# Performance work log

Hardware: AMD Instinct MI355X
Metric: run time of the kernel (lower is better)

Reference implementation:

```python
import jax, jax.numpy as jnp
import numpy as np

WIDTH = 66   # channel width; width*SX*SY == 2376 (hardcoded GRU input size)
SX, SY = 6, 6
MODES = 3
HID = 16     # GRU hidden; forced by self.out = Linear(16, 1)
FEAT = WIDTH * SX * SY  # 2376
EPS = 1e-5   # InstanceNorm2d eps


def _gelu(x):
    return jax.nn.gelu(x, approximate=False)  # torch default exact gelu


def _inorm(x):
    # InstanceNorm2d, affine=False, biased variance over spatial dims
    m = x.mean(axis=(-2, -1), keepdims=True)
    v = ((x - m) ** 2).mean(axis=(-2, -1), keepdims=True)
    return (x - m) * jax.lax.rsqrt(v + EPS)


def _conv1x1(x, w, b):
    # x: [n, ci, h, w], w: [co, ci], b: [co]
    return jnp.einsum('bixy,oi->boxy', x, w) + b[None, :, None, None]


def _mlp(x, wa, ba, wb, bb):
    return _conv1x1(_gelu(_conv1x1(x, wa, ba)), wb, bb)


def _spectral(x, w1r, w1i, w2r, w2i):
    # x: [n, c, SX, SY]
    w1 = w1r + 1j * w1i
    w2 = w2r + 1j * w2i
    xft = jnp.fft.rfft2(x)  # [n, c, SX, SY//2+1]
    o1 = jnp.einsum('bixy,ioxy->boxy', xft[:, :, :MODES, :MODES], w1)
    o2 = jnp.einsum('bixy,ioxy->boxy', xft[:, :, SX - MODES:, :MODES], w2)
    oft = jnp.zeros((x.shape[0], w1.shape[1], SX, SY // 2 + 1), dtype=xft.dtype)
    oft = oft.at[:, :, :MODES, :MODES].set(o1)
    oft = oft.at[:, :, SX - MODES:, :MODES].set(o2)
    return jnp.fft.irfft2(oft, s=(SX, SY))


def _gru_layer(x, wi, wh, bi, bh):
    # x: [T, B, I]; torch GRU gate order: r, z, n
    B = x.shape[1]
    H = wh.shape[1]

    def step(h, xt):
        gi = xt @ wi.T + bi
        gh = h @ wh.T + bh
        ir, iz, inn = jnp.split(gi, 3, axis=-1)
        hr, hz, hn = jnp.split(gh, 3, axis=-1)
        r = jax.nn.sigmoid(ir + hr)
        z = jax.nn.sigmoid(iz + hz)
        n = jnp.tanh(inn + r * hn)
        h_new = (1.0 - z) * n + z * h
        return h_new, h_new

    h0 = jnp.zeros((B, H), x.dtype)
    _, ys = jax.lax.scan(step, h0, x)
    return ys  # [T, B, H]


def setup_inputs() -> dict:
    key = jax.random.key(0)
    ks = iter(jax.random.split(key, 64))
    W = WIDTH
    scale = 1.0 / (W * W)

    def n(shape, s=0.02):
        return (jax.random.normal(next(ks), shape, dtype=jnp.float32) * s)

    def spec(shape):
        return scale * jax.random.uniform(next(ks), shape, dtype=jnp.float32)

    inp = {
        'X': jax.random.normal(next(ks), (64, 256, SX, SY), dtype=jnp.float32),
        'p_w': n((3, W), 0.3), 'p_b': n((W,)),
        'c0_w1r': spec((W, W, MODES, MODES)), 'c0_w1i': spec((W, W, MODES, MODES)),
        'c0_w2r': spec((W, W, MODES, MODES)), 'c0_w2i': spec((W, W, MODES, MODES)),
        'c1_w1r': spec((W, W, MODES, MODES)), 'c1_w1i': spec((W, W, MODES, MODES)),
        'c1_w2r': spec((W, W, MODES, MODES)), 'c1_w2i': spec((W, W, MODES, MODES)),
        'm0a_w': n((W, W)), 'm0a_b': n((W,)), 'm0b_w': n((W, W)), 'm0b_b': n((W,)),
        'm1a_w': n((W, W)), 'm1a_b': n((W,)), 'm1b_w': n((W, W)), 'm1b_b': n((W,)),
        'w0_w': n((W, W)), 'w0_b': n((W,)),
        'w1_w': n((W, W)), 'w1_b': n((W,)),
        'gru0_wi': n((3 * HID, FEAT)), 'gru0_wh': n((3 * HID, HID)),
        'gru0_bi': n((3 * HID,)), 'gru0_bh': n((3 * HID,)),
        'gru1_wi': n((3 * HID, HID)), 'gru1_wh': n((3 * HID, HID)),
        'gru1_bi': n((3 * HID,)), 'gru1_bh': n((3 * HID,)),
        'out_w': n((1, HID)), 'out_b': n((1,)),
    }
    return inp


def reference(X, p_w, p_b,
              c0_w1r, c0_w1i, c0_w2r, c0_w2i,
              c1_w1r, c1_w1i, c1_w2r, c1_w2i,
              m0a_w, m0a_b, m0b_w, m0b_b,
              m1a_w, m1a_b, m1b_w, m1b_b,
              w0_w, w0_b, w1_w, w1_b,
              gru0_wi, gru0_wh, gru0_bi, gru0_bh,
              gru1_wi, gru1_wh, gru1_bi, gru1_bh,
              out_w, out_b):
    B, T = X.shape[0], X.shape[1]
    N = B * T
    x = (X + 0.01).reshape(N, SX, SY)
    # grid channels (linspace 0..1)
    gx = jnp.broadcast_to(jnp.linspace(0.0, 1.0, SX, dtype=X.dtype)[None, :, None], (N, SX, SY))
    gy = jnp.broadcast_to(jnp.linspace(0.0, 1.0, SY, dtype=X.dtype)[None, None, :], (N, SX, SY))
    h = jnp.stack([x, gx, gy], axis=-1) @ p_w + p_b      # [N, SX, SY, W]
    h = jnp.transpose(h, (0, 3, 1, 2))                   # [N, W, SX, SY]

    def block(h, sc, mp, wc):
        y = _mlp(_inorm(_spectral(_inorm(h), *sc)), *mp)
        return _gelu(y + _conv1x1(h, *wc))

    h = block(h, (c0_w1r, c0_w1i, c0_w2r, c0_w2i), (m0a_w, m0a_b, m0b_w, m0b_b), (w0_w, w0_b))
    h = block(h, (c1_w1r, c1_w1i, c1_w2r, c1_w2i), (m1a_w, m1a_b, m1b_w, m1b_b), (w1_w, w1_b))

    feats = h.reshape(B, T, FEAT)                        # X_all, [B, T, 2376]
    seq = jnp.transpose(feats, (1, 0, 2))                # [T, B, 2376]
    seq = _gru_layer(seq, gru0_wi, gru0_wh, gru0_bi, gru0_bh)
    seq = _gru_layer(seq, gru1_wi, gru1_wh, gru1_bi, gru1_bh)
    y = jnp.transpose(seq, (1, 0, 2)) @ out_w.T + out_b  # [B, T, 1]
    return y
```

## Files before the change

kernel.cpp:

```cpp
#include <hip/hip_runtime.h>

#define NTH 320
#define SPB 4
#define W66 66
#define PIX36 36
#define NPOS 18
#define FEAT 2376
#define TT 256
#define NSAMP 16384
#define CHU (SPB * W66)
#define SROW 2376

#define PACK_FLOATS (2 * NPOS * W66 * W66)
#define C1P_OFF  PACK_FLOATS
#define C2P_OFF  (C1P_OFF + 11616)
#define GI0_OFF  (C2P_OFF + 23232)

static constexpr float KC[6] = {1.f, 0.5f, -0.5f, -1.f, -0.5f, 0.5f};
static constexpr float KS[6] = {0.f, 0.8660254037844386468f, 0.8660254037844386468f,
                                0.f, -0.8660254037844386468f, -0.8660254037844386468f};

__device__ __forceinline__ float gelu_f(float v) {
    return 0.5f * v * (1.f + erff(v * 0.70710678118654752440f));
}

__device__ __forceinline__ void load_row36(float* d, const float* p) {
    const float4* r = (const float4*)p;
    #pragma unroll
    for (int q = 0; q < 9; ++q) {
        float4 v = r[q];
        d[4*q] = v.x; d[4*q+1] = v.y; d[4*q+2] = v.z; d[4*q+3] = v.w;
    }
}

extern "C" __global__ void repack_kernel(
    const float* __restrict__ w1r0, const float* __restrict__ w1i0,
    const float* __restrict__ w2r0, const float* __restrict__ w2i0,
    const float* __restrict__ w1r1, const float* __restrict__ w1i1,
    const float* __restrict__ w2r1, const float* __restrict__ w2i1,
    const float* __restrict__ m0aw, const float* __restrict__ m1aw,
    const float* __restrict__ m0bw, const float* __restrict__ m1bw,
    const float* __restrict__ w0w,  const float* __restrict__ w1w,
    float* __restrict__ ws)
{
    int e = blockIdx.x * blockDim.x + threadIdx.x;
    const int TOT = 2 * NPOS * W66 * W66;
    if (e < TOT) {
        int L = e / (NPOS * W66 * W66);
        int r = e % (NPOS * W66 * W66);
        int p = r / (W66 * W66);
        int io = r % (W66 * W66);
        int i = io / W66, o = io % W66;
        int kx = p / 3, ky = p % 3;
        const float *wr, *wi;
        int kxw;
        if (L == 0) { if (kx < 3) { wr = w1r0; wi = w1i0; kxw = kx; } else { wr = w2r0; wi = w2i0; kxw = kx - 3; } }
        else        { if (kx < 3) { wr = w1r1; wi = w1i1; kxw = kx; } else { wr = w2r1; wi = w2i1; kxw = kx - 3; } }
        int src = ((i * W66 + o) * 3 + kxw) * 3 + ky;
        ws[(size_t)e * 2 + 0] = wr[src];
        ws[(size_t)e * 2 + 1] = wi[src];
    }
    if (e < 2 * 66 * 22) {
        int L = e / (66 * 22); int r = e % (66 * 22);
        int i = r / 22, cp = r % 22;
        const float* mw = L ? m1aw : m0aw;
        float4 v;
        v.x = mw[(3*cp + 0) * 66 + i];
        v.y = mw[(3*cp + 1) * 66 + i];
        v.z = mw[(3*cp + 2) * 66 + i];
        v.w = 0.f;
        ((float4*)(ws + C1P_OFF))[e] = v;
    }
    if (e < 2 * 66 * 22) {
        int L = e / (66 * 22); int r = e % (66 * 22);
        int i = r / 22, cp = r % 22;
        const float* mb = L ? m1bw : m0bw;
        const float* sk = L ? w1w : w0w;
        float4 a, b;
        a.x = mb[(3*cp + 0) * 66 + i]; a.y = mb[(3*cp + 1) * 66 + i];
        a.z = mb[(3*cp + 2) * 66 + i]; a.w = 0.f;
        b.x = sk[(3*cp + 0) * 66 + i]; b.y = sk[(3*cp + 1) * 66 + i];
        b.z = sk[(3*cp + 2) * 66 + i]; b.w = 0.f;
        ((float4*)(ws + C2P_OFF))[(size_t)e * 2 + 0] = a;
        ((float4*)(ws + C2P_OFF))[(size_t)e * 2 + 1] = b;
    }
}

extern "C" __global__ void __launch_bounds__(NTH, 2)
fno_kernel(const float* __restrict__ X, const float* __restrict__ p_w,
           const float* __restrict__ p_b, const float* __restrict__ ws,
           const float* __restrict__ m0ab, const float* __restrict__ m1ab,
           const float* __restrict__ m0bb, const float* __restrict__ m1bb,
           const float* __restrict__ w0b, const float* __restrict__ w1b,
           const float* __restrict__ gwi, const float* __restrict__ gbi,
           float* __restrict__ gi0out)
{
    extern __shared__ float sm[];
    float* A  = sm;
    float* Bb = sm + SPB * SROW;

    const int tid = threadIdx.x;
    const int n0 = blockIdx.x * SPB;
    const int s = tid & 3, ch = tid >> 2;
    const bool actC = tid < CHU;
    const int cs = tid & 3, ct = tid >> 2;
    const int chp = ct % 3, ccp = ct / 3;

    if (actC) {
        float h[36];
        float pw0 = p_w[ch], pw1 = p_w[66 + ch], pw2 = p_w[132 + ch], pb = p_b[ch];
        const float4* xr = (const float4*)(X + (size_t)(n0 + s) * 36);
        #pragma unroll
        for (int q = 0; q < 9; ++q) {
            float4 v = xr[q];
            float vv[4] = {v.x, v.y, v.z, v.w};
            #pragma unroll
            for (int e = 0; e < 4; ++e) {
                int pix = 4 * q + e;
                int px = pix / 6, py = pix % 6;
                h[pix] = fmaf(vv[e] + 0.01f, pw0,
                          fmaf(px * 0.2f, pw1, fmaf(py * 0.2f, pw2, pb)));
            }
        }
        float4* r = (float4*)(A + s * SROW + ch * 36);
        #pragma unroll
        for (int q = 0; q < 9; ++q)
            r[q] = make_float4(h[4*q], h[4*q+1], h[4*q+2], h[4*q+3]);
    }

    for (int L = 0; L < 2; ++L) {
        const float* mab = L ? m1ab : m0ab;
        const float* mbb = L ? m1bb : m0bb;
        const float* skb = L ? w1b : w0b;
        const float2* packL = ((const float2*)ws) + (size_t)L * NPOS * W66 * W66;
        const float4* c1p = (const float4*)(ws + C1P_OFF) + (size_t)L * 66 * 22;
        const float4* c2p = (const float4*)(ws + C2P_OFF) + (size_t)L * 66 * 22 * 2;

        if (actC) {
            float h[36];
            load_row36(h, A + s * SROW + ch * 36);
            float sum = 0.f, sq = 0.f;
            #pragma unroll
            for (int x = 0; x < 36; ++x) { sum += h[x]; sq = fmaf(h[x], h[x], sq); }
            float hm = sum * (1.f / 36.f);
            float hrs = rsqrtf(sq * (1.f / 36.f) - hm * hm + 1e-5f);
            float tr[6][3], ti[6][3];
            #pragma unroll
            for (int px = 0; px < 6; ++px) {
                float a0 = h[px*6+0], a1 = h[px*6+1], a2 = h[px*6+2];
                float a3 = h[px*6+3], a4 = h[px*6+4], a5 = h[px*6+5];
                float s14 = a1 + a4, d14 = a1 - a4, s25 = a2 + a5, d25 = a2 - a5;
                tr[px][0] = (a0 + a3) + s14 + s25;
                ti[px][0] = 0.f;
                tr[px][1] = (a0 - a3) + 0.5f * (d14 - d25);
                ti[px][1] = -0.8660254037844386468f * (d14 + d25);
                tr[px][2] = (a0 + a3) - 0.5f * (s14 + s25);
                ti[px][2] = -0.8660254037844386468f * (s14 - s25);
            }
            float2* xf = (float2*)Bb;
            #pragma unroll
            for (int kx = 0; kx < 6; ++kx) {
                #pragma unroll
                for (int ky = 0; ky < 3; ++ky) {
                    float xr = 0.f, xi = 0.f;
                    #pragma unroll
                    for (int px = 0; px < 6; ++px) {
                        const int m = (kx * px) % 6;
                        xr += tr[px][ky] * KC[m] + ti[px][ky] * KS[m];
                        xi += ti[px][ky] * KC[m] - tr[px][ky] * KS[m];
                    }
                    if (kx == 0 && ky == 0) xr -= 36.f * hm;
                    xf[((kx * 3 + ky) * 66 + ch) * 4 + s] = make_float2(hrs * xr, hrs * xi);
                }
            }
        }
        __syncthreads();

        {
            float ar0[4], ai0[4], br0[4], bi0[4];
            float ar1[4], ai1[4], br1[4], bi1[4];
            const bool a1 = (tid + NTH) < 594;
            int p0 = tid / 33, o0 = (tid - p0 * 33) * 2;
            int u1 = a1 ? (tid + NTH) : tid;
            int p1 = u1 / 33, o1 = (u1 - p1 * 33) * 2;
            {
                #pragma unroll
                for (int q = 0; q < 4; ++q) { ar0[q]=0.f; ai0[q]=0.f; br0[q]=0.f; bi0[q]=0.f; }
                const float2* xfp = (const float2*)Bb + (size_t)p0 * 264;
                const float2* wp = packL + (size_t)p0 * 66 * 66;
                #pragma unroll 3
                for (int i = 0; i < 66; ++i) {
                    const float4* xv = (const float4*)(xfp + i * 4);
                    float4 x0 = xv[0], x1 = xv[1];
                    float4 wv = *(const float4*)(wp + i * 66 + o0);
                    float xr[4] = {x0.x, x0.z, x1.x, x1.z};
                    float xi[4] = {x0.y, x0.w, x1.y, x1.w};
                    #pragma unroll
                    for (int q = 0; q < 4; ++q) {
                        ar0[q] = fmaf(xr[q], wv.x, ar0[q]); ar0[q] = fmaf(xi[q], -wv.y, ar0[q]);
                        ai0[q] = fmaf(xr[q], wv.y, ai0[q]); ai0[q] = fmaf(xi[q],  wv.x, ai0[q]);
                        br0[q] = fmaf(xr[q], wv.z, br0[q]); br0[q] = fmaf(xi[q], -wv.w, br0[q]);
                        bi0[q] = fmaf(xr[q], wv.w, bi0[q]); bi0[q] = fmaf(xi[q],  wv.z, bi0[q]);
                    }
                }
            }
            {
                #pragma unroll
                for (int q = 0; q < 4; ++q) { ar1[q]=0.f; ai1[q]=0.f; br1[q]=0.f; bi1[q]=0.f; }
                const float2* xfp = (const float2*)Bb + (size_t)p1 * 264;
                const float2* wp = packL + (size_t)p1 * 66 * 66;
                #pragma unroll 3
                for (int i = 0; i < 66; ++i) {
                    const float4* xv = (const float4*)(xfp + i * 4);
                    float4 x0 = xv[0], x1 = xv[1];
                    float4 wv = *(const float4*)(wp + i * 66 + o1);
                    float xr[4] = {x0.x, x0.z, x1.x, x1.z};
                    float xi[4] = {x0.y, x0.w, x1.y, x1.w};
                    #pragma unroll
                    for (int q = 0; q < 4; ++q) {
                        ar1[q] = fmaf(xr[q], wv.x, ar1[q]); ar1[q] = fmaf(xi[q], -wv.y, ar1[q]);
                        ai1[q] = fmaf(xr[q], wv.y, ai1[q]); ai1[q] = fmaf(xi[q],  wv.x, ai1[q]);
                        br1[q] = fmaf(xr[q], wv.z, br1[q]); br1[q] = fmaf(xi[q], -wv.w, br1[q]);
                        bi1[q] = fmaf(xr[q], wv.w, bi1[q]); bi1[q] = fmaf(xi[q],  wv.z, bi1[q]);
                    }
                }
            }
            __syncthreads();
            {
                float2* xf = (float2*)Bb;
                float4* d0 = (float4*)(xf + ((size_t)p0 * 66 + o0) * 4);
                float4* d1 = (float4*)(xf + ((size_t)p0 * 66 + o0 + 1) * 4);
                d0[0] = make_float4(ar0[0], ai0[0], ar0[1], ai0[1]);
                d0[1] = make_float4(ar0[2], ai0[2], ar0[3], ai0[3]);
                d1[0] = make_float4(br0[0], bi0[0], br0[1], bi0[1]);
                d1[1] = make_float4(br0[2], bi0[2], br0[3], bi0[3]);
                if (a1) {
                    float4* e0 = (float4*)(xf + ((size_t)p1 * 66 + o1) * 4);
                    float4* e1 = (float4*)(xf + ((size_t)p1 * 66 + o1 + 1) * 4);
                    e0[0] = make_float4(ar1[0], ai1[0], ar1[1], ai1[1]);
                    e0[1] = make_float4(ar1[2], ai1[2], ar1[3], ai1[3]);
                    e1[0] = make_float4(br1[0], bi1[0], br1[1], bi1[1]);
                    e1[1] = make_float4(br1[2], bi1[2], br1[3], bi1[3]);
                }
            }
        }
        __syncthreads();

        {
            float sp[36];
            if (actC) {
                const float2* xf = (const float2*)Bb;
                float ar0[6], ar1[6], ai1[6], ar2[6], ai2[6];
                #pragma unroll
                for (int px = 0; px < 6; ++px) {
                    ar0[px]=0.f; ar1[px]=0.f; ai1[px]=0.f; ar2[px]=0.f; ai2[px]=0.f;
                }
                #pragma unroll
                for (int kx = 0; kx < 6; ++kx) {
                    float2 o0 = xf[((kx * 3 + 0) * 66 + ch) * 4 + s];
                    float2 o1 = xf[((kx * 3 + 1) * 66 + ch) * 4 + s];
                    float2 o2 = xf[((kx * 3 + 2) * 66 + ch) * 4 + s];
                    #pragma unroll
                    for (int px = 0; px < 6; ++px) {
                        const int m = (kx * px) % 6;
                        ar0[px] += o0.x * KC[m] - o0.y * KS[m];
                        ar1[px] += o1.x * KC[m] - o1.y * KS[m];
                        ai1[px] += o1.x * KS[m] + o1.y * KC[m];
                        ar2[px] += o2.x * KC[m] - o2.y * KS[m];
                        ai2[px] += o2.x * KS[m] + o2.y * KC[m];
                    }
                }
                float sum = 0.f, sq = 0.f;
                #pragma unroll
                for (int px = 0; px < 6; ++px) {
                    #pragma unroll
                    for (int py = 0; py < 6; ++py) {
                        const int m2 = (2 * py) % 6;
                        float sv = (1.f/36.f) * ar0[px]
                                 + (1.f/18.f) * (ar1[px] * KC[py] - ai1[px] * KS[py])
                                 + (1.f/18.f) * (ar2[px] * KC[m2] - ai2[px] * KS[m2]);
                        sp[px*6+py] = sv; sum += sv; sq = fmaf(sv, sv, sq);
                    }
                }
                float m = sum * (1.f / 36.f);
                float rs = rsqrtf(sq * (1.f / 36.f) - m * m + 1e-5f);
                #pragma unroll
                for (int x = 0; x < 36; ++x) sp[x] = (sp[x] - m) * rs;
            }
            __syncthreads();
            if (actC) {
                float4* r = (float4*)(Bb + s * SROW + ch * 36);
                #pragma unroll
                for (int q = 0; q < 9; ++q)
                    r[q] = make_float4(sp[4*q], sp[4*q+1], sp[4*q+2], sp[4*q+3]);
            }
        }
        __syncthreads();

        {
            float acc[3][12];
            if (actC) {
                #pragma unroll
                for (int j = 0; j < 3; ++j)
                    #pragma unroll
                    for (int x = 0; x < 12; ++x) acc[j][x] = 0.f;
                #pragma unroll 4
                for (int i = 0; i < 66; ++i) {
                    float4 w = c1p[i * 22 + ccp];
                    const float4* xr = (const float4*)(Bb + cs * SROW + i * 36 + chp * 12);
                    #pragma unroll
                    for (int q = 0; q < 3; ++q) {
                        float4 v = xr[q];
                        float vv[4] = {v.x, v.y, v.z, v.w};
                        #pragma unroll
                        for (int e = 0; e < 4; ++e) {
                            acc[0][4*q+e] = fmaf(w.x, vv[e], acc[0][4*q+e]);
                            acc[1][4*q+e] = fmaf(w.y, vv[e], acc[1][4*q+e]);
                            acc[2][4*q+e] = fmaf(w.z, vv[e], acc[2][4*q+e]);
                        }
                    }
                }
                float b0 = mab[3*ccp], b1 = mab[3*ccp+1], b2 = mab[3*ccp+2];
                #pragma unroll
                for (int x = 0; x < 12; ++x) {
                    acc[0][x] = gelu_f(acc[0][x] + b0);
                    acc[1][x] = gelu_f(acc[1][x] + b1);
                    acc[2][x] = gelu_f(acc[2][x] + b2);
                }
            }
            __syncthreads();
            if (actC) {
                #pragma unroll
                for (int j = 0; j < 3; ++j) {
                    float4* dst = (float4*)(Bb + cs * SROW + (3*ccp+j) * 36 + chp * 12);
                    dst[0] = make_float4(acc[j][0], acc[j][1], acc[j][2],  acc[j][3]);
                    dst[1] = make_float4(acc[j][4], acc[j][5], acc[j][6],  acc[j][7]);
                    dst[2] = make_float4(acc[j][8], acc[j][9], acc[j][10], acc[j][11]);
                }
            }
        }
        __syncthreads();

        {
            float acc[3][12];
            if (actC) {
                #pragma unroll
                for (int j = 0; j < 3; ++j)
                    #pragma unroll
                    for (int x = 0; x < 12; ++x) acc[j][x] = 0.f;
                #pragma unroll 3
                for (int i = 0; i < 66; ++i) {
                    float4 wy = c2p[(i * 22 + ccp) * 2 + 0];
                    float4 wk = c2p[(i * 22 + ccp) * 2 + 1];
                    const float4* tr4 = (const float4*)(Bb + cs * SROW + i * 36 + chp * 12);
                    const float4* ar4 = (const float4*)(A  + cs * SROW + i * 36 + chp * 12);
                    #pragma unroll
                    for (int q = 0; q < 3; ++q) {
                        float4 tv = tr4[q], av = ar4[q];
                        float tvv[4] = {tv.x, tv.y, tv.z, tv.w};
                        float avv[4] = {av.x, av.y, av.z, av.w};
                        #pragma unroll
                        for (int e = 0; e < 4; ++e) {
                            acc[0][4*q+e] = fmaf(wy.x, tvv[e], fmaf(wk.x, avv[e], acc[0][4*q+e]));
                            acc[1][4*q+e] = fmaf(wy.y, tvv[e], fmaf(wk.y, avv[e], acc[1][4*q+e]));
                            acc[2][4*q+e] = fmaf(wy.z, tvv[e], fmaf(wk.z, avv[e], acc[2][4*q+e]));
                        }
                    }
                }
                #pragma unroll
                for (int j = 0; j < 3; ++j) {
                    float bj = mbb[3*ccp+j] + skb[3*ccp+j];
                    #pragma unroll
                    for (int x = 0; x < 12; ++x) acc[j][x] = gelu_f(acc[j][x] + bj);
                }
            }
            __syncthreads();
            if (actC) {
                #pragma unroll
                for (int j = 0; j < 3; ++j) {
                    float4* dst = (float4*)(A + cs * SROW + (3*ccp+j) * 36 + chp * 12);
                    dst[0] = make_float4(acc[j][0], acc[j][1], acc[j][2],  acc[j][3]);
                    dst[1] = make_float4(acc[j][4], acc[j][5], acc[j][6],  acc[j][7]);
                    dst[2] = make_float4(acc[j][8], acc[j][9], acc[j][10], acc[j][11]);
                }
            }
        }
        __syncthreads();
    }

    #pragma unroll
    for (int rnd = 0; rnd < 2; ++rnd) {
        int u = tid + rnd * NTH;
        if (u < 576) {
            int third = u / 192, sg = u - third * 192;
            int es = sg & 3, g = sg >> 2;
            const float* ab = A + es * SROW + third * 792;
            const float* wb = gwi + (size_t)g * FEAT + third * 792;
            float a0 = 0.f, a1 = 0.f, a2 = 0.f, a3 = 0.f;
            #pragma unroll 2
            for (int w = 0; w < 22; ++w) {
                const float4* ar4 = (const float4*)(ab + w * 36);
                const float4* wr4 = (const float4*)(wb + w * 36);
                #pragma unroll
                for (int q = 0; q < 9; ++q) {
                    float4 av = ar4[q], wv = wr4[q];
                    a0 = fmaf(av.x, wv.x, a0); a1 = fmaf(av.y, wv.y, a1);
                    a2 = fmaf(av.z, wv.z, a2); a3 = fmaf(av.w, wv.w, a3);
                }
            }
            Bb[u] = (a0 + a1) + (a2 + a3);
        }
    }
    __syncthreads();
    if (tid < 192) {
        int es = tid & 3, g = tid >> 2;
        gi0out[(size_t)(n0 + es) * 48 + g] = Bb[tid] + Bb[tid + 192] + Bb[tid + 384] + gbi[g];
    }
}

extern "C" __global__ void __launch_bounds__(64, 1)
gru_kernel(const float* __restrict__ gi0, const float* __restrict__ wh0,
           const float* __restrict__ bh0, const float* __restrict__ wi1,
           const float* __restrict__ wh1, const float* __restrict__ bi1,
           const float* __restrict__ bh1, const float* __restrict__ outw,
           const float* __restrict__ outb, float* __restrict__ y)
{
    int b = blockIdx.x;
    int g = threadIdx.x;
    int gw = (g < 48) ? g : 0;
    float rwh0[16], rwi1[16], rwh1[16];
    #pragma unroll
    for (int j = 0; j < 16; ++j) {
        rwh0[j] = wh0[gw * 16 + j];
        rwi1[j] = wi1[gw * 16 + j];
        rwh1[j] = wh1[gw * 16 + j];
    }
    float vbh0 = bh0[gw], vbi1 = bi1[gw], vbh1 = bh1[gw];
    float vow = (g < 16) ? outw[g] : 0.f;
    float ob = outb[0];
    float h0 = 0.f, h1 = 0.f;
    int base = b * TT;
    int j = g & 15;
    float cur = (g < 48) ? gi0[(size_t)base * 48 + g] : 0.f;
    for (int t = 0; t < TT; ++t) {
        int tn = (t + 1 < TT) ? t + 1 : t;
        float nxt = (g < 48) ? gi0[((size_t)base + tn) * 48 + g] : 0.f;
        float gh0 = vbh0;
        #pragma unroll
        for (int k = 0; k < 16; ++k) gh0 = fmaf(rwh0[k], __shfl(h0, k), gh0);
        float gir = __shfl(cur, j), giz = __shfl(cur, 16 + j), gin = __shfl(cur, 32 + j);
        float ghr = __shfl(gh0, j), ghz = __shfl(gh0, 16 + j), ghn = __shfl(gh0, 32 + j);
        float r = 1.f / (1.f + expf(-(gir + ghr)));
        float z = 1.f / (1.f + expf(-(giz + ghz)));
        float n = tanhf(gin + r * ghn);
        h0 = (1.f - z) * n + z * h0;
        float gi1 = vbi1, gh1 = vbh1;
        #pragma unroll
        for (int k = 0; k < 16; ++k) {
            gi1 = fmaf(rwi1[k], __shfl(h0, k), gi1);
            gh1 = fmaf(rwh1[k], __shfl(h1, k), gh1);
        }
        float air = __shfl(gi1, j) + __shfl(gh1, j);
        float aiz = __shfl(gi1, 16 + j) + __shfl(gh1, 16 + j);
        float r1 = 1.f / (1.f + expf(-air));
        float z1 = 1.f / (1.f + expf(-aiz));
        float n1 = tanhf(__shfl(gi1, 32 + j) + r1 * __shfl(gh1, 32 + j));
        h1 = (1.f - z1) * n1 + z1 * h1;
        float v = h1 * vow;
        #pragma unroll
        for (int off = 32; off; off >>= 1) v += __shfl_xor(v, off);
        if (g == 0) y[base + t] = v + ob;
        cur = nxt;
    }
}

extern "C" void kernel_launch(void* const* d_in, const int* in_sizes, int n_in,
                              void* d_out, int out_size, void* d_ws, size_t ws_size,
                              hipStream_t stream) {
    const float* X    = (const float*)d_in[0];
    const float* p_w  = (const float*)d_in[1];
    const float* p_b  = (const float*)d_in[2];
    const float* c0w1r = (const float*)d_in[3];
    const float* c0w1i = (const float*)d_in[4];
    const float* c0w2r = (const float*)d_in[5];
    const float* c0w2i = (const float*)d_in[6];
    const float* c1w1r = (const float*)d_in[7];
    const float* c1w1i = (const float*)d_in[8];
    const float* c1w2r = (const float*)d_in[9];
    const float* c1w2i = (const float*)d_in[10];
    const float* m0aw = (const float*)d_in[11];
    const float* m0ab = (const float*)d_in[12];
    const float* m0bw = (const float*)d_in[13];
    const float* m0bb = (const float*)d_in[14];
    const float* m1aw = (const float*)d_in[15];
    const float* m1ab = (const float*)d_in[16];
    const float* m1bw = (const float*)d_in[17];
    const float* m1bb = (const float*)d_in[18];
    const float* w0w  = (const float*)d_in[19];
    const float* w0b  = (const float*)d_in[20];
    const float* w1w  = (const float*)d_in[21];
    const float* w1b  = (const float*)d_in[22];
    const float* g0wi = (const float*)d_in[23];
    const float* g0wh = (const float*)d_in[24];
    const float* g0bi = (const float*)d_in[25];
    const float* g0bh = (const float*)d_in[26];
    const float* g1wi = (const float*)d_in[27];
    const float* g1wh = (const float*)d_in[28];
    const float* g1bi = (const float*)d_in[29];
    const float* g1bh = (const float*)d_in[30];
    const float* outw = (const float*)d_in[31];
    const float* outb = (const float*)d_in[32];
    float* out = (float*)d_out;

    float* ws   = (float*)d_ws;
    float* gi0  = ws + GI0_OFF;

    repack_kernel<<<(2 * NPOS * W66 * W66 + 255) / 256, 256, 0, stream>>>(
        c0w1r, c0w1i, c0w2r, c0w2i, c1w1r, c1w1i, c1w2r, c1w2i,
        m0aw, m1aw, m0bw, m1bw, w0w, w1w, ws);

    size_t lds = (size_t)(2 * SPB * SROW) * sizeof(float);
    hipFuncSetAttribute(reinterpret_cast<const void*>(fno_kernel),
                        hipFuncAttributeMaxDynamicSharedMemorySize, (int)lds);
    fno_kernel<<<NSAMP / SPB, NTH, lds, stream>>>(
        X, p_w, p_b, ws,
        m0ab, m1ab, m0bb, m1bb, w0b, w1b,
        g0wi, g0bi, gi0);

    gru_kernel<<<64, 64, 0, stream>>>(gi0, g0wh, g0bh, g1wi, g1wh, g1bi, g1bh, outw, outb, out);
}
```

Before: 1.910 ms.

## Use four LDS regions to drop intra-stage barriers in FNO kernel

Gives the fused FNO kernel four shared-memory buffers instead of two and rotates the roles (skip input, spectrum, mode output, normalized, MLP hidden, block output) across them. Because each stage now writes to a different region than it reads, the __syncthreads between compute and write-back inside each stage can be removed. Several loop unroll factors are also raised. LDS use per block doubles to about 152 KB, which at two blocks per CU under the launch bounds would exceed the LDS available and likely halve occupancy. The normalized-write code also contains a redundant odd expression that is then overwritten.

Measured after the change: 2.119 ms. 11.0% more time.

```diff
diff --git a/kernel.cpp b/kernel.cpp
--- a/kernel.cpp
+++ b/kernel.cpp
@@ -10,6 +10,7 @@
 #define NSAMP 16384
 #define CHU (SPB * W66)
 #define SROW 2376
+#define REG  (SPB * SROW)
 
 #define PACK_FLOATS (2 * NPOS * W66 * W66)
 #define C1P_OFF  PACK_FLOATS
@@ -96,8 +97,10 @@
            float* __restrict__ gi0out)
 {
     extern __shared__ float sm[];
-    float* A  = sm;
-    float* Bb = sm + SPB * SROW;
+    float* R0 = sm;
+    float* R1 = sm + REG;
+    float* R2 = sm + 2 * REG;
+    float* R3 = sm + 3 * REG;
 
     const int tid = threadIdx.x;
     const int n0 = blockIdx.x * SPB;
@@ -122,7 +125,7 @@
                           fmaf(px * 0.2f, pw1, fmaf(py * 0.2f, pw2, pb)));
             }
         }
-        float4* r = (float4*)(A + s * SROW + ch * 36);
+        float4* r = (float4*)(R0 + s * SROW + ch * 36);
         #pragma unroll
         for (int q = 0; q < 9; ++q)
             r[q] = make_float4(h[4*q], h[4*q+1], h[4*q+2], h[4*q+3]);
@@ -136,9 +139,16 @@
         const float4* c1p = (const float4*)(ws + C1P_OFF) + (size_t)L * 66 * 22;
         const float4* c2p = (const float4*)(ws + C2P_OFF) + (size_t)L * 66 * 22 * 2;
 
+        float* Askip = L ? R2 : R0;
+        float* Fx    = L ? R0 : R1;
+        float* Mo    = L ? R1 : R2;
+        float* Ir    = R3;
+        float* Ct    = L ? R0 : R1;
+        float* Cout  = L ? R1 : R2;
+
         if (actC) {
             float h[36];
-            load_row36(h, A + s * SROW + ch * 36);
+            load_row36(h, Askip + s * SROW + ch * 36);
             float sum = 0.f, sq = 0.f;
             #pragma unroll
             for (int x = 0; x < 36; ++x) { sum += h[x]; sq = fmaf(h[x], h[x], sq); }
@@ -157,7 +167,7 @@
                 tr[px][2] = (a0 + a3) - 0.5f * (s14 + s25);
                 ti[px][2] = -0.8660254037844386468f * (s14 - s25);
             }
-            float2* xf = (float2*)Bb;
+            float2* xf = (float2*)Fx;
             #pragma unroll
             for (int kx = 0; kx < 6; ++kx) {
                 #pragma unroll
@@ -186,9 +196,9 @@
             {
                 #pragma unroll
                 for (int q = 0; q < 4; ++q) { ar0[q]=0.f; ai0[q]=0.f; br0[q]=0.f; bi0[q]=0.f; }
-                const float2* xfp = (const float2*)Bb + (size_t)p0 * 264;
+                const float2* xfp = (const float2*)Fx + (size_t)p0 * 264;
                 const float2* wp = packL + (size_t)p0 * 66 * 66;
-                #pragma unroll 3
+                #pragma unroll 4
                 for (int i = 0; i < 66; ++i) {
                     const float4* xv = (const float4*)(xfp + i * 4);
                     float4 x0 = xv[0], x1 = xv[1];
@@ -207,9 +217,9 @@
             {
                 #pragma unroll
                 for (int q = 0; q < 4; ++q) { ar1[q]=0.f; ai1[q]=0.f; br1[q]=0.f; bi1[q]=0.f; }
-                const float2* xfp = (const float2*)Bb + (size_t)p1 * 264;
+                const float2* xfp = (const float2*)Fx + (size_t)p1 * 264;
                 const float2* wp = packL + (size_t)p1 * 66 * 66;
-                #pragma unroll 3
+                #pragma unroll 4
                 for (int i = 0; i < 66; ++i) {
                     const float4* xv = (const float4*)(xfp + i * 4);
                     float4 x0 = xv[0], x1 = xv[1];
@@ -225,9 +235,8 @@
                     }
                 }
             }
-            __syncthreads();
             {
-                float2* xf = (float2*)Bb;
+                float2* xf = (float2*)Mo;
                 float4* d0 = (float4*)(xf + ((size_t)p0 * 66 + o0) * 4);
                 float4* d1 = (float4*)(xf + ((size_t)p0 * 66 + o0 + 1) * 4);
                 d0[0] = make_float4(ar0[0], ai0[0], ar0[1], ai0[1]);
@@ -246,54 +255,53 @@
         }
         __syncthreads();
 
-        {
+        if (actC) {
             float sp[36];
-            if (actC) {
-                const float2* xf = (const float2*)Bb;
-                float ar0[6], ar1[6], ai1[6], ar2[6], ai2[6];
+            const float2* xf = (const float2*)Mo;
+            float ar0[6], ar1[6], ai1[6], ar2[6], ai2[6];
+            #pragma unroll
+            for (int px = 0; px < 6; ++px) {
+                ar0[px]=0.f; ar1[px]=0.f; ai1[px]=0.f; ar2[px]=0.f; ai2[px]=0.f;
+            }
+            #pragma unroll
+            for (int kx = 0; kx < 6; ++kx) {
+                float2 o0 = xf[((kx * 3 + 0) * 66 + ch) * 4 + s];
+                float2 o1 = xf[((kx * 3 + 1) * 66 + ch) * 4 + s];
+                float2 o2 = xf[((kx * 3 + 2) * 66 + ch) * 4 + s];
                 #pragma unroll
                 for (int px = 0; px < 6; ++px) {
-                    ar0[px]=0.f; ar1[px]=0.f; ai1[px]=0.f; ar2[px]=0.f; ai2[px]=0.f;
-                }
-                #pragma unroll
-                for (int kx = 0; kx < 6; ++kx) {
-                    float2 o0 = xf[((kx * 3 + 0) * 66 + ch) * 4 + s];
-                    float2 o1 = xf[((kx * 3 + 1) * 66 + ch) * 4 + s];
-                    float2 o2 = xf[((kx * 3 + 2) * 66 + ch) * 4 + s];
-                    #pragma unroll
-                    for (int px = 0; px < 6; ++px) {
-                        const int m = (kx * px) % 6;
-                        ar0[px] += o0.x * KC[m] - o0.y * KS[m];
-                        ar1[px] += o1.x * KC[m] - o1.y * KS[m];
-                        ai1[px] += o1.x * KS[m] + o1.y * KC[m];
-                        ar2[px] += o2.x * KC[m] - o2.y * KS[m];
-                        ai2[px] += o2.x * KS[m] + o2.y * KC[m];
-                    }
-                }
-                float sum = 0.f, sq = 0.f;
-                #pragma unroll
-                for (int px = 0; px < 6; ++px) {
-                    #pragma unroll
-                    for (int py = 0; py < 6; ++py) {
-                        const int m2 = (2 * py) % 6;
-                        float sv = (1.f/36.f) * ar0[px]
-                                 + (1.f/18.f) * (ar1[px] * KC[py] - ai1[px] * KS[py])
-                                 + (1.f/18.f) * (ar2[px] * KC[m2] - ai2[px] * KS[m2]);
-                        sp[px*6+py] = sv; sum += sv; sq = fmaf(sv, sv, sq);
-                    }
-                }
-                float m = sum * (1.f / 36.f);
-                float rs = rsqrtf(sq * (1.f / 36.f) - m * m + 1e-5f);
-                #pragma unroll
-                for (int x = 0; x < 36; ++x) sp[x] = (sp[x] - m) * rs;
-            }
-            __syncthreads();
-            if (actC) {
-                float4* r = (float4*)(Bb + s * SROW + ch * 36);
-                #pragma unroll
-                for (int q = 0; q < 9; ++q)
-                    r[q] = make_float4(sp[4*q], sp[4*q+1], sp[4*q+2], sp[4*q+3]);
-            }
+                    const int m = (kx * px) % 6;
+                    ar0[px] += o0.x * KC[m] - o0.y * KS[m];
+                    ar1[px] += o1.x * KC[m] - o1.y * KS[m];
+                    ai1[px] += o1.x * KS[m] + o1.y * KC[m];
+                    ar2[px] += o2.x * KC[m] - o2.y * KS[m];
+                    ai2[px] += o2.x * KS[m] + o2.y * KC[m];
+                }
+            }
+            float sum = 0.f, sq = 0.f;
+            #pragma unroll
+            for (int px = 0; px < 6; ++px) {
+                #pragma unroll
+                for (int py = 0; py < 6; ++py) {
+                    const int m2 = (2 * py) % 6;
+                    float sv = (1.f/36.f) * ar0[px]
+                             + (1.f/18.f) * (ar1[px] * KC[py] - ai1[px] * KS[py])
+                             + (1.f/18.f) * (ar2[px] * KC[m2] - ai2[px] * KS[m2]);
+                    sp[px*6+py] = sv; sum += sv; sq = fmaf(sv, sv, sq);
+                }
+            }
+            float m = sum * (1.f / 36.f);
+            float rs = rsqrtf(sq * (1.f / 36.f) - m * m + 1e-5f);
+            float4* r = (float4*)(Ir + s * SROW + ch * 36);
+            #pragma unroll
+            for (int q = 0; q < 9; ++q)
+                r[q] = make_float4((sp[4*q+0]-0.f)*rs - m*rs + (sp[4*q+0]-sp[4*q+0]),
+                                   (sp[4*q+1]-m)*rs, (sp[4*q+2]-m)*rs, (sp[4*q+3]-m)*rs);
+            r[0].x = (sp[0]-m)*rs; r[0].y = (sp[1]-m)*rs; r[0].z = (sp[2]-m)*rs; r[0].w = (sp[3]-m)*rs;
+            #pragma unroll
+            for (int q = 1; q < 9; ++q)
+                r[q] = make_float4((sp[4*q+0]-m)*rs, (sp[4*q+1]-m)*rs,
+                                   (sp[4*q+2]-m)*rs, (sp[4*q+3]-m)*rs);
         }
         __syncthreads();
 
@@ -304,10 +312,10 @@
                 for (int j = 0; j < 3; ++j)
                     #pragma unroll
                     for (int x = 0; x < 12; ++x) acc[j][x] = 0.f;
-                #pragma unroll 4
+                #pragma unroll 6
                 for (int i = 0; i < 66; ++i) {
                     float4 w = c1p[i * 22 + ccp];
-                    const float4* xr = (const float4*)(Bb + cs * SROW + i * 36 + chp * 12);
+                    const float4* xr = (const float4*)(Ir + cs * SROW + i * 36 + chp * 12);
                     #pragma unroll
                     for (int q = 0; q < 3; ++q) {
                         float4 v = xr[q];
@@ -327,12 +335,9 @@
                     acc[1][x] = gelu_f(acc[1][x] + b1);
                     acc[2][x] = gelu_f(acc[2][x] + b2);
                 }
-            }
-            __syncthreads();
-            if (actC) {
                 #pragma unroll
                 for (int j = 0; j < 3; ++j) {
-                    float4* dst = (float4*)(Bb + cs * SROW + (3*ccp+j) * 36 + chp * 12);
+                    float4* dst = (float4*)(Ct + cs * SROW + (3*ccp+j) * 36 + chp * 12);
                     dst[0] = make_float4(acc[j][0], acc[j][1], acc[j][2],  acc[j][3]);
                     dst[1] = make_float4(acc[j][4], acc[j][5], acc[j][6],  acc[j][7]);
                     dst[2] = make_float4(acc[j][8], acc[j][9], acc[j][10], acc[j][11]);
@@ -348,12 +353,12 @@
                 for (int j = 0; j < 3; ++j)
                     #pragma unroll
                     for (int x = 0; x < 12; ++x) acc[j][x] = 0.f;
-                #pragma unroll 3
+                #pragma unroll 4
                 for (int i = 0; i < 66; ++i) {
                     float4 wy = c2p[(i * 22 + ccp) * 2 + 0];
                     float4 wk = c2p[(i * 22 + ccp) * 2 + 1];
-                    const float4* tr4 = (const float4*)(Bb + cs * SROW + i * 36 + chp * 12);
-                    const float4* ar4 = (const float4*)(A  + cs * SROW + i * 36 + chp * 12);
+                    const float4* tr4 = (const float4*)(Ct + cs * SROW + i * 36 + chp * 12);
+                    const float4* ar4 = (const float4*)(Askip + cs * SROW + i * 36 + chp * 12);
                     #pragma unroll
                     for (int q = 0; q < 3; ++q) {
                         float4 tv = tr4[q], av = ar4[q];
@@ -373,12 +378,9 @@
                     #pragma unroll
                     for (int x = 0; x < 12; ++x) acc[j][x] = gelu_f(acc[j][x] + bj);
                 }
-            }
-            __syncthreads();
-            if (actC) {
                 #pragma unroll
                 for (int j = 0; j < 3; ++j) {
-                    float4* dst = (float4*)(A + cs * SROW + (3*ccp+j) * 36 + chp * 12);
+                    float4* dst = (float4*)(Cout + cs * SROW + (3*ccp+j) * 36 + chp * 12);
                     dst[0] = make_float4(acc[j][0], acc[j][1], acc[j][2],  acc[j][3]);
                     dst[1] = make_float4(acc[j][4], acc[j][5], acc[j][6],  acc[j][7]);
                     dst[2] = make_float4(acc[j][8], acc[j][9], acc[j][10], acc[j][11]);
@@ -394,7 +396,7 @@
         if (u < 576) {
             int third = u / 192, sg = u - third * 192;
             int es = sg & 3, g = sg >> 2;
-            const float* ab = A + es * SROW + third * 792;
+            const float* ab = R1 + es * SROW + third * 792;
             const float* wb = gwi + (size_t)g * FEAT + third * 792;
             float a0 = 0.f, a1 = 0.f, a2 = 0.f, a3 = 0.f;
             #pragma unroll 2
@@ -408,13 +410,13 @@
                     a2 = fmaf(av.z, wv.z, a2); a3 = fmaf(av.w, wv.w, a3);
                 }
             }
-            Bb[u] = (a0 + a1) + (a2 + a3);
+            R0[u] = (a0 + a1) + (a2 + a3);
         }
     }
     __syncthreads();
     if (tid < 192) {
         int es = tid & 3, g = tid >> 2;
-        gi0out[(size_t)(n0 + es) * 48 + g] = Bb[tid] + Bb[tid + 192] + Bb[tid + 384] + gbi[g];
+        gi0out[(size_t)(n0 + es) * 48 + g] = R0[tid] + R0[tid + 192] + R0[tid + 384] + gbi[g];
     }
 }
 
@@ -519,7 +521,7 @@
         c0w1r, c0w1i, c0w2r, c0w2i, c1w1r, c1w1i, c1w2r, c1w2i,
         m0aw, m1aw, m0bw, m1bw, w0w, w1w, ws);
 
-    size_t lds = (size_t)(2 * SPB * SROW) * sizeof(float);
+    size_t lds = (size_t)(4 * REG) * sizeof(float);
     hipFuncSetAttribute(reinterpret_cast<const void*>(fno_kernel),
                         hipFuncAttributeMaxDynamicSharedMemorySize, (int)lds);
     fno_kernel<<<NSAMP / SPB, NTH, lds, stream>>>(
```
